# Optimization experiments

Hardware: AMD Instinct MI355X
Metric: run time of the kernel (lower is better)

Reference implementation:

```python
import jax, jax.numpy as jnp
import numpy as np

N_FEAT = 256
B, T = 8, 2048


def setup_inputs() -> dict:
    key = jax.random.key(0)
    k1, k2, k3, k4, k5, k6 = jax.random.split(key, 6)
    feat = jax.random.normal(k1, (B, T, N_FEAT), dtype=jnp.float32)
    hlens = jax.random.randint(k2, (B,), 1, T + 1, dtype=jnp.int32)
    # torch nn.Linear params: weight [out, in], bias [out]
    lim = 1.0 / np.sqrt(N_FEAT)
    Wq = jax.random.uniform(k3, (N_FEAT, N_FEAT), jnp.float32, -lim, lim)
    bq = jax.random.uniform(k4, (N_FEAT,), jnp.float32, -lim, lim)
    Wk = jax.random.uniform(k5, (N_FEAT, N_FEAT), jnp.float32, -lim, lim)
    bk = jax.random.uniform(k6, (N_FEAT,), jnp.float32, -lim, lim)
    return {"feat": feat, "hlens": hlens, "Wq": Wq, "bq": bq, "Wk": Wk, "bk": bk}


def reference(feat, hlens, Wq, bq, Wk, bk):
    # q/k projections (torch Linear: x @ W^T + b)
    q = jnp.einsum('btf,gf->btg', feat, Wq) + bq  # [B, T, F]
    k = jnp.einsum('btf,gf->btg', feat, Wk) + bk  # [B, T, F]
    sa = jnp.einsum('btf,bsf->bts', q, k)         # [B, T, T] full score matrix
    score = jnp.mean(sa, axis=-1)                 # [B, T]
    attn = jax.nn.softmax(sa, axis=-1)            # [B, T, T]
    feat_new = jnp.einsum('bts,bsf->btf', attn, feat)  # [B, T, F]
    # peaks is overwritten to all-True in the original, so hlens_new = T and
    # the per-batch gather loop is an identity copy -> feat_new unchanged.
    hlens_new = jnp.full((feat.shape[0],), feat.shape[1], dtype=jnp.int32)
    return feat_new, hlens_new, score
```

## Files before the change

kernel.cpp:

```cpp
#include <hip/hip_runtime.h>
#include <math.h>

#define B_ 8
#define T_ 2048
#define F_ 256
#define M_TOT (B_ * T_)

typedef __attribute__((ext_vector_type(8))) short short8;
typedef __attribute__((ext_vector_type(4))) float floatx4;

__device__ __forceinline__ short f2bf(float x) {
    unsigned u = __float_as_uint(x);
    u += 0x7FFF + ((u >> 16) & 1);
    return (short)(u >> 16);
}
__device__ __forceinline__ float bf2f(short s) {
    return __uint_as_float(((unsigned)(unsigned short)s) << 16);
}

__device__ __forceinline__ void cp_g2l_16(const void* g, void* l) {
    __builtin_amdgcn_global_load_lds(
        (const __attribute__((address_space(1))) void*)g,
        (__attribute__((address_space(3))) void*)l, 16, 0, 0);
}

__global__ __launch_bounds__(256) void pack_feat_all(
    const float* __restrict__ feat,
    short* __restrict__ featAh, short* __restrict__ featAl,
    short* __restrict__ stg, float* __restrict__ featpart,
    const float* __restrict__ Wq, const float* __restrict__ Wk,
    short* __restrict__ wfqh, short* __restrict__ wfql,
    short* __restrict__ wfkh)
{
    const int tid = threadIdx.x;
    const int lane = tid & 63, w = tid >> 6;
    const int quad = lane >> 4, l15 = lane & 15;

    if (blockIdx.x == 64) {
#pragma unroll
        for (int i = 0; i < 8; ++i) {
            const int idx = blockIdx.y * 32 + w * 8 + i;
            const int isk = idx >> 7, nt = (idx >> 3) & 15, fc = idx & 7;
            const float* __restrict__ W = isk ? Wk : Wq;
            const int row = nt * 16 + l15, col = fc * 32 + quad * 8;
            float v[8];
            *(float4*)&v[0] = *(const float4*)&W[(size_t)row * F_ + col];
            *(float4*)&v[4] = *(const float4*)&W[(size_t)row * F_ + col + 4];
            const size_t dst = ((size_t)(nt * 8 + fc)) * 512 + lane * 8;
            if (isk) {
                short8 h;
#pragma unroll
                for (int j = 0; j < 8; ++j) h[j] = f2bf(v[j]);
                *(short8*)&wfkh[dst] = h;
            } else {
                short8 h, l;
#pragma unroll
                for (int j = 0; j < 8; ++j) {
                    const short hh = f2bf(v[j]);
                    h[j] = hh; l[j] = f2bf(v[j] - bf2f(hh));
                }
                *(short8*)&wfqh[dst] = h;
                *(short8*)&wfql[dst] = l;
            }
        }
        return;
    }

    __shared__ float lds[32][260];
    const int kc  = blockIdx.x;
    const int b   = blockIdx.y;

#pragma unroll
    for (int i = 0; i < 8; ++i) {
        const int lin = i * 256 + tid;
        const int r = lin >> 6, c4 = (lin & 63) * 4;
        float4 v = *(const float4*)&feat[((size_t)b * T_ + kc * 32 + r) * F_ + c4];
        lds[r][c4 + 0] = v.x; lds[r][c4 + 1] = v.y;
        lds[r][c4 + 2] = v.z; lds[r][c4 + 3] = v.w;
    }
    __syncthreads();

#pragma unroll
    for (int i = 0; i < 4; ++i) {
        const int idx = w * 4 + i;
        const int r16h = idx >> 3, fc = idx & 7;
        float v[8];
        *(float4*)&v[0] = *(const float4*)&lds[r16h * 16 + l15][fc * 32 + quad * 8];
        *(float4*)&v[4] = *(const float4*)&lds[r16h * 16 + l15][fc * 32 + quad * 8 + 4];
        short8 h, l;
#pragma unroll
        for (int j = 0; j < 8; ++j) {
            const short hh = f2bf(v[j]);
            h[j] = hh; l[j] = f2bf(v[j] - bf2f(hh));
        }
        const int r16 = b * 128 + kc * 2 + r16h;
        const size_t dst = ((size_t)r16 * 8 + fc) * 512 + lane * 8;
        __builtin_nontemporal_store(h, (short8*)&featAh[dst]);
        __builtin_nontemporal_store(l, (short8*)&featAl[dst]);
    }

#pragma unroll
    for (int fi = 0; fi < 4; ++fi) {
        const int ft = w + fi * 4;
        short8 h;
#pragma unroll
        for (int j = 0; j < 8; ++j)
            h[j] = f2bf(lds[quad * 8 + j][ft * 16 + l15]);
        const size_t dst = ((size_t)(b * 64 + kc)) * 16384 + 8192 + ft * 512 + lane * 8;
        *(short8*)&stg[dst] = h;
    }

    {
        float s = 0.f;
#pragma unroll
        for (int r = 0; r < 32; ++r) s += lds[r][tid];
        featpart[((size_t)b * 64 + kc) * 256 + tid] = s;
    }
}

__global__ __launch_bounds__(256) void wvec_kernel(
    const float* __restrict__ featpart,
    const float* __restrict__ Wq, const float* __restrict__ bq,
    const float* __restrict__ Wk, const float* __restrict__ bk,
    float* __restrict__ wv, float* __restrict__ cv,
    float* __restrict__ out_hlens)
{
    __shared__ float fb[256];
    __shared__ float kb[256];
    const int b = blockIdx.x, tid = threadIdx.x;

    float s = 0.f;
#pragma unroll 8
    for (int c = 0; c < 64; ++c) s += featpart[((size_t)b * 64 + c) * 256 + tid];
    fb[tid] = s * (1.0f / (float)T_);
    __syncthreads();

    float acc = bk[tid];
#pragma unroll 8
    for (int f = 0; f < 256; ++f) acc += Wk[(size_t)tid * 256 + f] * fb[f];
    kb[tid] = acc;
    __syncthreads();

    float wf_ = 0.f;
#pragma unroll 8
    for (int g = 0; g < 256; ++g) wf_ += Wq[(size_t)g * 256 + tid] * kb[g];
    wv[b * 256 + tid] = wf_;

    __syncthreads();
    fb[tid] = bq[tid] * kb[tid];
    __syncthreads();
    for (int st = 128; st > 0; st >>= 1) {
        if (tid < st) fb[tid] += fb[tid + st];
        __syncthreads();
    }
    if (tid == 0) cv[b] = fb[0];
    if (b == 0 && tid < B_) out_hlens[tid] = (float)T_;
}

__global__ __launch_bounds__(256) void score_kernel(
    const float* __restrict__ feat, const float* __restrict__ wv,
    const float* __restrict__ cv, float* __restrict__ out_score)
{
    __shared__ float wl[256];
    const int tid = threadIdx.x;
    const int b   = blockIdx.x >> 5;
    const int t0s = (blockIdx.x & 31) * 64;
    wl[tid] = wv[b * 256 + tid];
    __syncthreads();

    const int row = t0s + (tid >> 2);
    const int fq  = (tid & 3) * 64;
    const float* fr = &feat[((size_t)b * T_ + row) * F_ + fq];
    float s = 0.f;
#pragma unroll
    for (int i = 0; i < 16; ++i) {
        float4 v = *(const float4*)&fr[i * 4];
        s += v.x * wl[fq + i * 4 + 0] + v.y * wl[fq + i * 4 + 1]
           + v.z * wl[fq + i * 4 + 2] + v.w * wl[fq + i * 4 + 3];
    }
    s += __shfl_xor(s, 1, 64);
    s += __shfl_xor(s, 2, 64);
    if ((tid & 3) == 0) out_score[(size_t)b * T_ + row] = s + cv[b];
}

__global__ __launch_bounds__(512, 4) void proj_mfma(
    const short* __restrict__ featAh, const short* __restrict__ featAl,
    const short* __restrict__ wfqh, const short* __restrict__ wfql,
    const short* __restrict__ wfkh,
    const float* __restrict__ bq, const float* __restrict__ bk,
    short* __restrict__ qfh, short* __restrict__ qfl,
    short* __restrict__ stg)
{
    __shared__ short wbuf[2][8192];
    __shared__ float Tr[8][16][36];

    const int tid = threadIdx.x, lane = tid & 63, w = tid >> 6;
    const int quad = lane >> 4, l15 = lane & 15;
    const int x  = blockIdx.x;
    const int ng = x & 3, rg = x >> 2;
    const bool isq = ng < 2;
    const int r16 = rg * 8 + w;
    const int b = r16 >> 7, qt16 = r16 & 127;
    const int ntb = isq ? ng * 8 : (ng - 2) * 8;

    short8 ah[8], al[8];
#pragma unroll
    for (int fc = 0; fc < 8; ++fc) {
        const size_t off = ((size_t)r16 * 8 + fc) * 512 + lane * 8;
        ah[fc] = *(const short8*)&featAh[off];
        al[fc] = *(const short8*)&featAl[off];
    }

    const short* __restrict__ wsh = (isq ? wfqh : wfkh) + (size_t)ntb * 4096;
    const short* __restrict__ wsl = wfql + (size_t)ntb * 4096;
    const float* __restrict__ bias = isq ? bq : bk;

    cp_g2l_16(wsh + tid * 8, &wbuf[0][tid * 8]);
    if (isq) cp_g2l_16(wsl + tid * 8, &wbuf[0][4096 + tid * 8]);

    int cur = 0;
    for (int i = 0; i < 8; ++i, cur ^= 1) {
        __syncthreads();

        floatx4 C = (floatx4){0.f, 0.f, 0.f, 0.f};
#pragma unroll
        for (int fc = 0; fc < 8; ++fc) {
            short8 wh = *(const short8*)&wbuf[cur][fc * 512 + lane * 8];
            C = __builtin_amdgcn_mfma_f32_16x16x32_bf16(ah[fc], wh, C, 0, 0, 0);
            C = __builtin_amdgcn_mfma_f32_16x16x32_bf16(al[fc], wh, C, 0, 0, 0);
            if (isq) {
                short8 wl2 = *(const short8*)&wbuf[cur][4096 + fc * 512 + lane * 8];
                C = __builtin_amdgcn_mfma_f32_16x16x32_bf16(ah[fc], wl2, C, 0, 0, 0);
            }
        }

        if (i + 1 < 8) {
            cp_g2l_16(wsh + (size_t)(i + 1) * 4096 + tid * 8,
                      &wbuf[cur ^ 1][tid * 8]);
            if (isq) cp_g2l_16(wsl + (size_t)(i + 1) * 4096 + tid * 8,
                               &wbuf[cur ^ 1][4096 + tid * 8]);
        }

        const int nt = ntb + i;
        const float bv = bias[nt * 16 + l15];
        const int ch = (i & 1) * 16;
#pragma unroll
        for (int r = 0; r < 4; ++r)
            Tr[w][quad * 4 + r][ch + l15] = C[r] + bv;

        if (i & 1) {
            float v[8];
            *(float4*)&v[0] = *(const float4*)&Tr[w][l15][quad * 8];
            *(float4*)&v[4] = *(const float4*)&Tr[w][l15][quad * 8 + 4];
            const int p = nt >> 1;
            if (isq) {
                short8 h, l;
#pragma unroll
                for (int j = 0; j < 8; ++j) {
                    const short hh = f2bf(v[j]);
                    h[j] = hh; l[j] = f2bf(v[j] - bf2f(hh));
                }
                const size_t dst = ((size_t)(b * 8 + p) * 128 + qt16) * 512 + lane * 8;
                __builtin_nontemporal_store(h, (short8*)&qfh[dst]);
                __builtin_nontemporal_store(l, (short8*)&qfl[dst]);
            } else {
                short8 h;
#pragma unroll
                for (int j = 0; j < 8; ++j) h[j] = f2bf(v[j]);
                const size_t dst = ((size_t)(b * 64 + (qt16 >> 1))) * 16384
                                 + (p * 2 + (qt16 & 1)) * 512 + lane * 8;
                *(short8*)&stg[dst] = h;
            }
        }
    }
}

__global__ __launch_bounds__(256, 2) void attn_mfma(
    const short* __restrict__ qfh_g, const short* __restrict__ qfl_g,
    const short* __restrict__ stg,
    float* __restrict__ o0, float* __restrict__ o1,
    float* __restrict__ lpart)
{
    __shared__ short kbuf[2][16384];
    __shared__ float P_lds[64 * 36];
    __shared__ float l_lds[2][64];

    const int tid  = threadIdx.x;
    const int wave = tid >> 6, lane = tid & 63;
    const int qp   = wave & 1, fh = wave >> 1;
    const int quad = lane >> 4, l15 = lane & 15;

    const int lid  = blockIdx.x;
    const int b    = lid & 7;
    const int qt   = (lid >> 3) & 31;
    const int ks   = lid >> 8;

    short8 qh[2][8], ql[2][8];
#pragma unroll
    for (int t = 0; t < 2; ++t) {
        const int qt16 = qt * 4 + qp * 2 + t;
#pragma unroll
        for (int fc = 0; fc < 8; ++fc) {
            const size_t off = ((size_t)(b * 8 + fc) * 128 + qt16) * 512 + lane * 8;
            qh[t][fc] = *(const short8*)&qfh_g[off];
            ql[t][fc] = *(const short8*)&qfl_g[off];
        }
    }

    floatx4 O[2][8];
#pragma unroll
    for (int t = 0; t < 2; ++t)
#pragma unroll
        for (int i = 0; i < 8; ++i) O[t][i] = (floatx4){0.f, 0.f, 0.f, 0.f};
    float lsum[2][4] = {};

    const short* sbase = &stg[(size_t)b * 64 * 16384];
    const int kbeg = ks * 32, kend = kbeg + 32;

    {
        const short* src = sbase + (size_t)kbeg * 16384 + tid * 8;
        short* dst = &kbuf[0][tid * 8];
#pragma unroll
        for (int i = 0; i < 8; ++i)
            cp_g2l_16(src + i * 2048, dst + i * 2048);
    }

    int cur = 0;
    for (int kt = kbeg; kt < kend; ++kt, cur ^= 1) {
        __syncthreads();

        if (kt + 1 < kend) {
            const short* src = sbase + (size_t)(kt + 1) * 16384 + tid * 8;
            short* dst = &kbuf[cur ^ 1][tid * 8];
#pragma unroll
            for (int i = 0; i < 8; ++i)
                cp_g2l_16(src + i * 2048, dst + i * 2048);
        }

        floatx4 S[2];
#pragma unroll
        for (int t = 0; t < 2; ++t) S[t] = (floatx4){0.f, 0.f, 0.f, 0.f};
#pragma unroll
        for (int fc = 0; fc < 8; ++fc) {
            short8 bh = *(const short8*)&kbuf[cur][(fc * 2 + fh) * 512 + lane * 8];
#pragma unroll
            for (int t = 0; t < 2; ++t) {
                S[t] = __builtin_amdgcn_mfma_f32_16x16x32_bf16(qh[t][fc], bh, S[t], 0, 0, 0);
                S[t] = __builtin_amdgcn_mfma_f32_16x16x32_bf16(ql[t][fc], bh, S[t], 0, 0, 0);
            }
        }

#pragma unroll
        for (int t = 0; t < 2; ++t)
#pragma unroll
            for (int r = 0; r < 4; ++r) {
                const float e = __expf(S[t][r]);
                lsum[t][r] += e;
                P_lds[((qp * 2 + t) * 16 + quad * 4 + r) * 36 + fh * 16 + l15] = e;
            }

        asm volatile("s_waitcnt lgkmcnt(0)" ::: "memory");
        __builtin_amdgcn_s_barrier();
        asm volatile("" ::: "memory");
        __builtin_amdgcn_sched_barrier(0);

        short8 ph[2];
#pragma unroll
        for (int t = 0; t < 2; ++t) {
            float pv[8];
            *(float4*)&pv[0] = *(const float4*)&P_lds[((qp * 2 + t) * 16 + l15) * 36 + quad * 8];
            *(float4*)&pv[4] = *(const float4*)&P_lds[((qp * 2 + t) * 16 + l15) * 36 + quad * 8 + 4];
#pragma unroll
            for (int j = 0; j < 8; ++j)
                ph[t][j] = f2bf(pv[j]);
        }

#pragma unroll
        for (int ft = 0; ft < 8; ++ft) {
            short8 fv = *(const short8*)&kbuf[cur][8192 + (fh * 8 + ft) * 512 + lane * 8];
#pragma unroll
            for (int t = 0; t < 2; ++t)
                O[t][ft] = __builtin_amdgcn_mfma_f32_16x16x32_bf16(ph[t], fv, O[t][ft], 0, 0, 0);
        }
    }

#pragma unroll
    for (int t = 0; t < 2; ++t)
#pragma unroll
        for (int r = 0; r < 4; ++r) {
            lsum[t][r] += __shfl_xor(lsum[t][r], 1, 64);
            lsum[t][r] += __shfl_xor(lsum[t][r], 2, 64);
            lsum[t][r] += __shfl_xor(lsum[t][r], 4, 64);
            lsum[t][r] += __shfl_xor(lsum[t][r], 8, 64);
        }
    if (l15 == 0) {
#pragma unroll
        for (int t = 0; t < 2; ++t)
#pragma unroll
            for (int r = 0; r < 4; ++r)
                l_lds[fh][(qp * 2 + t) * 16 + quad * 4 + r] = lsum[t][r];
    }
    __syncthreads();

    float* __restrict__ opart = ks ? o1 : o0;
    const size_t row0 = (size_t)b * T_ + qt * 64;

    if (tid < 64)
        __builtin_nontemporal_store(l_lds[0][tid] + l_lds[1][tid],
                                    &lpart[(size_t)ks * M_TOT + row0 + tid]);

#pragma unroll
    for (int t = 0; t < 2; ++t)
#pragma unroll
        for (int r = 0; r < 4; ++r) {
            const int qr = (qp * 2 + t) * 16 + quad * 4 + r;
#pragma unroll
            for (int ft = 0; ft < 8; ++ft)
                __builtin_nontemporal_store(
                    O[t][ft][r],
                    &opart[(row0 + qr) * F_ + fh * 128 + ft * 16 + l15]);
        }
}

__global__ __launch_bounds__(256) void combine_kernel(
    float* __restrict__ out_feat, const float* __restrict__ o1,
    const float* __restrict__ lpart)
{
    const size_t gid = (size_t)blockIdx.x * 256 + threadIdx.x;
    const size_t row = gid >> 6;
    const float inv = 1.0f / (lpart[row] + lpart[M_TOT + row]);
    floatx4 a  = __builtin_nontemporal_load(&((const floatx4*)out_feat)[gid]);
    floatx4 bx = __builtin_nontemporal_load(&((const floatx4*)o1)[gid]);
    a = (a + bx) * inv;
    __builtin_nontemporal_store(a, &((floatx4*)out_feat)[gid]);
}

extern "C" void kernel_launch(void* const* d_in, const int* in_sizes, int n_in,
                              void* d_out, int out_size, void* d_ws, size_t ws_size,
                              hipStream_t stream)
{
    const float* feat = (const float*)d_in[0];
    const float* Wq = (const float*)d_in[2];
    const float* bq = (const float*)d_in[3];
    const float* Wk = (const float*)d_in[4];
    const float* bk = (const float*)d_in[5];

    float* out_feat  = (float*)d_out;
    float* out_hlens = out_feat + (size_t)M_TOT * F_;
    float* out_score = out_hlens + B_;

    short* featAh = (short*)d_ws;
    short* featAl = featAh + (size_t)M_TOT * F_;
    short* qfh    = featAl + (size_t)M_TOT * F_;
    short* qfl    = qfh + (size_t)M_TOT * F_;
    short* stg    = qfl + (size_t)M_TOT * F_;
    short* wfqh   = stg + (size_t)2 * M_TOT * F_;
    short* wfql   = wfqh + 65536;
    short* wfkh   = wfql + 65536;
    float* featpart = (float*)(wfkh + 65536);
    float* wv     = featpart + 131072;
    float* cv     = wv + 2048;
    float* o1     = (float*)featAh;
    float* lpart  = featpart;

    dim3 fgrid(65, B_);
    pack_feat_all<<<fgrid, 256, 0, stream>>>(feat, featAh, featAl, stg, featpart,
                                             Wq, Wk, wfqh, wfql, wfkh);

    wvec_kernel<<<B_, 256, 0, stream>>>(featpart, Wq, bq, Wk, bk, wv, cv, out_hlens);

    score_kernel<<<256, 256, 0, stream>>>(feat, wv, cv, out_score);

    proj_mfma<<<512, 512, 0, stream>>>(featAh, featAl, wfqh, wfql, wfkh,
                                       bq, bk, qfh, qfl, stg);

    attn_mfma<<<512, 256, 0, stream>>>(qfh, qfl, stg, out_feat, o1, lpart);

    combine_kernel<<<M_TOT * F_ / 4 / 256, 256, 0, stream>>>(out_feat, o1, lpart);
}
```

Measured before the change: 197.9 us.

## Software-pipeline attention PV with previous tile and double 128-row blocks

The attention kernel now uses 512-thread blocks that cover 128 query rows each, halving the grid so every streamed K/feat tile is shared by twice as many rows. The loop is software-pipelined: the P·V MFMAs for the previous tile run after the QK scores of the current tile, using a triple-buffered K/feat LDS ring and double-buffered P tiles. This removes the mid-iteration barrier between the exp write and the P read. In exchange the block uses more LDS, runs at one block per CU, and needs an epilogue for the last tile.

```diff
diff --git a/kernel.cpp b/kernel.cpp
--- a/kernel.cpp
+++ b/kernel.cpp
@@ -275,30 +275,30 @@
     }
 }
 
-__global__ __launch_bounds__(256, 2) void attn_mfma(
+__global__ __launch_bounds__(512, 1) void attn_mfma(
     const short* __restrict__ qfh_g, const short* __restrict__ qfl_g,
     const short* __restrict__ stg,
     float* __restrict__ o0, float* __restrict__ o1,
     float* __restrict__ lpart)
 {
-    __shared__ short kbuf[2][16384];
-    __shared__ float P_lds[64 * 36];
-    __shared__ float l_lds[2][64];
+    __shared__ short kbuf[3][16384];
+    __shared__ float P_lds[2][128 * 36];
+    __shared__ float l_lds[2][128];
 
     const int tid  = threadIdx.x;
     const int wave = tid >> 6, lane = tid & 63;
-    const int qp   = wave & 1, fh = wave >> 1;
+    const int qp   = wave & 3, fh = wave >> 2;
     const int quad = lane >> 4, l15 = lane & 15;
 
     const int lid  = blockIdx.x;
     const int b    = lid & 7;
-    const int qt   = (lid >> 3) & 31;
-    const int ks   = lid >> 8;
+    const int qg   = (lid >> 3) & 15;
+    const int ks   = lid >> 7;
 
     short8 qh[2][8], ql[2][8];
 #pragma unroll
     for (int t = 0; t < 2; ++t) {
-        const int qt16 = qt * 4 + qp * 2 + t;
+        const int qt16 = qg * 8 + qp * 2 + t;
 #pragma unroll
         for (int fc = 0; fc < 8; ++fc) {
             const size_t off = ((size_t)(b * 8 + fc) * 128 + qt16) * 512 + lane * 8;
@@ -319,22 +319,24 @@
 
     {
         const short* src = sbase + (size_t)kbeg * 16384 + tid * 8;
-        short* dst = &kbuf[0][tid * 8];
-#pragma unroll
-        for (int i = 0; i < 8; ++i)
-            cp_g2l_16(src + i * 2048, dst + i * 2048);
+#pragma unroll
+        for (int i = 0; i < 4; ++i)
+            cp_g2l_16(src + i * 4096, &kbuf[0][i * 4096 + tid * 8]);
     }
 
     int cur = 0;
-    for (int kt = kbeg; kt < kend; ++kt, cur ^= 1) {
+    for (int kt = kbeg; kt < kend; ++kt) {
+        const int prev = (cur == 0) ? 2 : cur - 1;
+        const int nxt  = (cur == 2) ? 0 : cur + 1;
+        const int par  = (kt - kbeg) & 1;
+
         __syncthreads();
 
         if (kt + 1 < kend) {
             const short* src = sbase + (size_t)(kt + 1) * 16384 + tid * 8;
-            short* dst = &kbuf[cur ^ 1][tid * 8];
-#pragma unroll
-            for (int i = 0; i < 8; ++i)
-                cp_g2l_16(src + i * 2048, dst + i * 2048);
+#pragma unroll
+            for (int i = 0; i < 4; ++i)
+                cp_g2l_16(src + i * 4096, &kbuf[nxt][i * 4096 + tid * 8]);
         }
 
         floatx4 S[2];
@@ -350,34 +352,58 @@
             }
         }
 
+        short8 ph[2];
+        if (kt > kbeg) {
+            const int ppar = par ^ 1;
+#pragma unroll
+            for (int t = 0; t < 2; ++t) {
+                float pv[8];
+                *(float4*)&pv[0] = *(const float4*)&P_lds[ppar][((qp * 2 + t) * 16 + l15) * 36 + quad * 8];
+                *(float4*)&pv[4] = *(const float4*)&P_lds[ppar][((qp * 2 + t) * 16 + l15) * 36 + quad * 8 + 4];
+#pragma unroll
+                for (int j = 0; j < 8; ++j)
+                    ph[t][j] = f2bf(pv[j]);
+            }
+        }
+
 #pragma unroll
         for (int t = 0; t < 2; ++t)
 #pragma unroll
             for (int r = 0; r < 4; ++r) {
                 const float e = __expf(S[t][r]);
                 lsum[t][r] += e;
-                P_lds[((qp * 2 + t) * 16 + quad * 4 + r) * 36 + fh * 16 + l15] = e;
-            }
-
-        asm volatile("s_waitcnt lgkmcnt(0)" ::: "memory");
-        __builtin_amdgcn_s_barrier();
-        asm volatile("" ::: "memory");
-        __builtin_amdgcn_sched_barrier(0);
-
+                P_lds[par][((qp * 2 + t) * 16 + quad * 4 + r) * 36 + fh * 16 + l15] = e;
+            }
+
+        if (kt > kbeg) {
+#pragma unroll
+            for (int ft = 0; ft < 8; ++ft) {
+                short8 fv = *(const short8*)&kbuf[prev][8192 + (fh * 8 + ft) * 512 + lane * 8];
+#pragma unroll
+                for (int t = 0; t < 2; ++t)
+                    O[t][ft] = __builtin_amdgcn_mfma_f32_16x16x32_bf16(ph[t], fv, O[t][ft], 0, 0, 0);
+            }
+        }
+        cur = nxt;
+    }
+
+    __syncthreads();
+    {
+        const int prev = (cur == 0) ? 2 : cur - 1;
+        const int ppar = (kend - 1 - kbeg) & 1;
         short8 ph[2];
 #pragma unroll
         for (int t = 0; t < 2; ++t) {
             float pv[8];
-            *(float4*)&pv[0] = *(const float4*)&P_lds[((qp * 2 + t) * 16 + l15) * 36 + quad * 8];
-            *(float4*)&pv[4] = *(const float4*)&P_lds[((qp * 2 + t) * 16 + l15) * 36 + quad * 8 + 4];
+            *(float4*)&pv[0] = *(const float4*)&P_lds[ppar][((qp * 2 + t) * 16 + l15) * 36 + quad * 8];
+            *(float4*)&pv[4] = *(const float4*)&P_lds[ppar][((qp * 2 + t) * 16 + l15) * 36 + quad * 8 + 4];
 #pragma unroll
             for (int j = 0; j < 8; ++j)
                 ph[t][j] = f2bf(pv[j]);
         }
-
 #pragma unroll
         for (int ft = 0; ft < 8; ++ft) {
-            short8 fv = *(const short8*)&kbuf[cur][8192 + (fh * 8 + ft) * 512 + lane * 8];
+            short8 fv = *(const short8*)&kbuf[prev][8192 + (fh * 8 + ft) * 512 + lane * 8];
 #pragma unroll
             for (int t = 0; t < 2; ++t)
                 O[t][ft] = __builtin_amdgcn_mfma_f32_16x16x32_bf16(ph[t], fv, O[t][ft], 0, 0, 0);
@@ -403,9 +429,9 @@
     __syncthreads();
 
     float* __restrict__ opart = ks ? o1 : o0;
-    const size_t row0 = (size_t)b * T_ + qt * 64;
-
-    if (tid < 64)
+    const size_t row0 = (size_t)b * T_ + qg * 128;
+
+    if (tid < 128)
         __builtin_nontemporal_store(l_lds[0][tid] + l_lds[1][tid],
                                     &lpart[(size_t)ks * M_TOT + row0 + tid]);
 
@@ -474,7 +500,7 @@
     proj_mfma<<<512, 512, 0, stream>>>(featAh, featAl, wfqh, wfql, wfkh,
                                        bq, bk, qfh, qfl, stg);
 
-    attn_mfma<<<512, 256, 0, stream>>>(qfh, qfl, stg, out_feat, o1, lpart);
+    attn_mfma<<<256, 512, 0, stream>>>(qfh, qfl, stg, out_feat, o1, lpart);
 
     combine_kernel<<<M_TOT * F_ / 4 / 256, 256, 0, stream>>>(out_feat, o1, lpart);
 }
```

Result: no change. 200.8 us (+1.5%).
